# Optimization experiments

Measured on AMD Instinct MI355X. Metric: run time of the kernel, lower is better.

The kernel has to match this reference:

```python
import jax, jax.numpy as jnp
import numpy as np

N_NODES = 100000
N_EDGES = 1600000
D = 128  # conv_channels = [128, 128, 128] -> two GCNConv layers


def setup_inputs() -> dict:
    key = jax.random.key(0)
    ks = jax.random.split(key, 6)
    x = jax.random.normal(ks[0], (N_NODES, D), dtype=jnp.float32)
    edge_index = jax.random.randint(ks[1], (2, N_EDGES), 0, N_NODES, dtype=jnp.int32)
    s = 1.0 / np.sqrt(D)
    W1 = jax.random.uniform(ks[2], (D, D), jnp.float32, -s, s)
    b1 = jnp.zeros((D,), jnp.float32)
    W2 = jax.random.uniform(ks[3], (D, D), jnp.float32, -s, s)
    b2 = jnp.zeros((D,), jnp.float32)
    return {"x": x, "edge_index": edge_index, "W1": W1, "b1": b1, "W2": W2, "b2": b2}


def _gcn_layer(x, W, b, src, dst, norm, n_nodes):
    h = x @ W                       # [N, out]
    msg = h[src] * norm[:, None]    # gather + scale, [E', out]
    agg = jax.ops.segment_sum(msg, dst, num_segments=n_nodes)
    return agg + b


def reference(x, edge_index, W1, b1, W2, b2):
    n = x.shape[0]
    # add_self_loops: append (i, i) for every node
    loop = jnp.arange(n, dtype=edge_index.dtype)
    src = jnp.concatenate([edge_index[0], loop])
    dst = jnp.concatenate([edge_index[1], loop])
    # symmetric GCN normalization: deg over target nodes (unit edge weights)
    deg = jax.ops.segment_sum(jnp.ones_like(src, dtype=x.dtype), dst, num_segments=n)
    dis = jnp.where(deg > 0, jax.lax.rsqrt(deg), 0.0)
    norm = dis[src] * dis[dst]      # [E']

    h = _gcn_layer(x, W1, b1, src, dst, norm, n)
    h = jax.nn.elu(h)
    # dropout p=0.3 is identity in eval mode
    h = _gcn_layer(h, W2, b2, src, dst, norm, n)
    h = jax.nn.elu(h)
    return h
```

## Files before the change

### kernel.cpp

```cpp
#include <hip/hip_runtime.h>
#include <math.h>

#define NN 100000
#define NE 1600000
#define NT (NE + NN)
#define DD 128
#define NB 500
#define BR 200
#define BCAP 4096
#define NCH 2048
#define NBK 782
#define NBG 1563
#define BMAGIC 21474837u

typedef unsigned int uint;
typedef unsigned short ushort;
typedef __attribute__((ext_vector_type(8))) short bf16x8;
typedef __attribute__((ext_vector_type(4))) float f32x4;

__device__ __forceinline__ uint bfr(float f){
  uint u = __float_as_uint(f);
  return (u + 0x7FFFu + ((u >> 16) & 1u)) >> 16;
}
__device__ __forceinline__ uint pk2(float a, float b){
  return (bfr(a) & 0xFFFFu) | (bfr(b) << 16);
}
__device__ __forceinline__ bf16x8 asbf(uint4 u){
  union { uint4 u; bf16x8 b; } c; c.u = u; return c.b;
}


__global__ __launch_bounds__(256) void k_bucket(const int* __restrict__ ei,
    int* __restrict__ gcnt, uint* __restrict__ bedge){
  __shared__ uint   ent[NCH];
  __shared__ ushort bbs[NCH];
  __shared__ int    hist[NB];
  __shared__ int    fl[NB];
  __shared__ int    gb[NB];
  int t = threadIdx.x;
  int base = blockIdx.x * NCH;
  int nv = NE - base; if (nv > NCH) nv = NCH;
  for (int b = t; b < NB; b += 256){ hist[b] = 0; fl[b] = 0; }
  __syncthreads();
  for (int j = t; j < nv; j += 256){
    int i = base + j;
    uint s = (uint)ei[i];
    uint d = (uint)ei[NE + i];
    uint b = __umulhi(d, BMAGIC);
    uint dl = d - b*BR;
    ent[j] = s | (dl << 17);
    bbs[j] = (ushort)b;
    atomicAdd(&hist[b], 1);
  }
  __syncthreads();
  for (int b = t; b < NB; b += 256){
    int h = hist[b];
    gb[b] = h ? atomicAdd(&gcnt[b*16], h) : 0;
  }
  __syncthreads();
  for (int j = t; j < nv; j += 256){
    uint b = bbs[j];
    int q = atomicAdd(&fl[b], 1);
    bedge[(size_t)b*BCAP + gb[b] + q] = ent[j];
  }
}

__global__ __launch_bounds__(512) void k_bscan(const int* __restrict__ gcnt, int* __restrict__ bbase){
  __shared__ int s[512];
  int t = threadIdx.x;
  int v = (t < NB) ? (gcnt[t*16] + BR) : 0;
  s[t] = v;
  __syncthreads();
  for (int off = 1; off < 512; off <<= 1){
    int a = (t >= off) ? s[t-off] : 0;
    __syncthreads();
    s[t] += a;
    __syncthreads();
  }
  if (t < NB) bbase[t] = s[t] - v;
}

__global__ __launch_bounds__(256) void k_build(const int* __restrict__ gcnt,
    const int* __restrict__ bbase, const uint* __restrict__ bedge,
    float* __restrict__ dis, int* __restrict__ rowptr, uint* __restrict__ es){
  __shared__ uint eL[BCAP];
  __shared__ int  cl[BR];
  __shared__ int  fl[BR];
  __shared__ int  pf[256];
  int b = blockIdx.x, t = threadIdx.x;
  int base = bbase[b];
  if (t < BR){ cl[t] = 0; fl[t] = 0; }
  __syncthreads();
  int cnt = gcnt[b*16];
  for (int e = t; e < cnt; e += 256){
    uint u = bedge[(size_t)b*BCAP + e];
    eL[e] = u;
    atomicAdd(&cl[u >> 17], 1);
  }
  __syncthreads();
  int v = (t < BR) ? (cl[t] + 1) : 0;
  pf[t] = v;
  __syncthreads();
  for (int off = 1; off < 256; off <<= 1){
    int a = (t >= off) ? pf[t-off] : 0;
    __syncthreads();
    pf[t] += a;
    __syncthreads();
  }
  if (t < BR){
    int n  = b*BR + t;
    int p0 = base + pf[t] - v;
    rowptr[n] = p0;
    dis[n] = rsqrtf((float)(cl[t] + 1));
    es[p0 + cl[t]] = (uint)n;
  }
  if (b == NB-1 && t == 0) rowptr[NN] = NT;
  __syncthreads();
  for (int e = t; e < cnt; e += 256){
    uint u = eL[e];
    int  dloc = u >> 17;
    int  q  = atomicAdd(&fl[dloc], 1);
    int  p0 = base + pf[dloc] - (cl[dloc] + 1);
    es[p0 + q] = u & 0x1FFFFu;
  }
}

__global__ __launch_bounds__(256) void k_wt(const float* __restrict__ W1f, const float* __restrict__ W2f,
    uint* __restrict__ Wt1, uint* __restrict__ Wt2){
  const float* W = blockIdx.x ? W2f : W1f;
  uint* Wt = blockIdx.x ? Wt2 : Wt1;
  int t = threadIdx.x;
  int n = t >> 1, k0 = (t & 1) * 64;
  for (int kk = 0; kk < 64; kk += 2){
    float v0 = W[(size_t)(k0+kk  )*DD + n];
    float v1 = W[(size_t)(k0+kk+1)*DD + n];
    Wt[(size_t)n*64 + ((k0+kk)>>1)] = pk2(v0, v1);
  }
}

template<int IN_BF16>
__global__ __launch_bounds__(256) void k_gemm(const void* __restrict__ Xv,
    const uint* __restrict__ Wt, const float* __restrict__ dis,
    uint* __restrict__ Y, int nrows){
  int t = threadIdx.x;
  int wv = t >> 6, l = t & 63;
  int g = l >> 4, li = l & 15;
  int r = blockIdx.x*64 + wv*16 + li;
  bool valid = (r < nrows);

  f32x4 acc[8];
  #pragma unroll
  for (int i = 0; i < 8; ++i) acc[i] = (f32x4){0.f,0.f,0.f,0.f};

  #pragma unroll
  for (int ks = 0; ks < 4; ++ks){
    int k0 = ks*32 + g*8;
    uint4 xb;
    if (IN_BF16){
      xb = valid ? ((const uint4*)Xv)[(size_t)r*16 + (k0>>3)] : make_uint4(0,0,0,0);
    } else {
      if (valid){
        const float* X = (const float*)Xv;
        float4 f0 = ((const float4*)X)[(size_t)r*32 + (k0>>2)];
        float4 f1 = ((const float4*)X)[(size_t)r*32 + (k0>>2) + 1];
        xb.x = pk2(f0.x, f0.y); xb.y = pk2(f0.z, f0.w);
        xb.z = pk2(f1.x, f1.y); xb.w = pk2(f1.z, f1.w);
      } else xb = make_uint4(0,0,0,0);
    }
    bf16x8 bfrag = asbf(xb);
    #pragma unroll
    for (int nt = 0; nt < 8; ++nt){
      uint4 wa = ((const uint4*)Wt)[(size_t)(nt*16 + li)*16 + (k0>>3)];
      acc[nt] = __builtin_amdgcn_mfma_f32_16x16x32_bf16(asbf(wa), bfrag, acc[nt], 0, 0, 0);
    }
  }
  if (valid){
    float dr = dis[r];
    #pragma unroll
    for (int nt = 0; nt < 8; ++nt){
      uint2 o;
      o.x = pk2(acc[nt][0]*dr, acc[nt][1]*dr);
      o.y = pk2(acc[nt][2]*dr, acc[nt][3]*dr);
      *(uint2*)&Y[(size_t)r*64 + nt*8 + g*2] = o;
    }
  }
}

template<int OUT_BF16>
__global__ __launch_bounds__(256) void k_agg(const uint* __restrict__ H,
    const int* __restrict__ rowptr, const float* __restrict__ dis,
    const uint* __restrict__ es, const float* __restrict__ bias,
    void* __restrict__ outv){
  int wid  = threadIdx.x >> 6;
  int lane = threadIdx.x & 63;
  int n = blockIdx.x*4 + wid;
  int e0 = rowptr[n];
  int e1 = rowptr[n+1];
  float a0 = 0.f, a1 = 0.f, a2 = 0.f, a3 = 0.f;
  int e = e0;

#define ASTEP(k,A,B) { uint s##k = es[e+k]; \
    uint h##k = H[(size_t)s##k*64 + lane]; \
    A += __uint_as_float(h##k << 16); \
    B += __uint_as_float(h##k & 0xFFFF0000u); }

  for (; e + 16 <= e1; e += 16){
    ASTEP( 0,a0,a1) ASTEP( 1,a2,a3) ASTEP( 2,a0,a1) ASTEP( 3,a2,a3)
    ASTEP( 4,a0,a1) ASTEP( 5,a2,a3) ASTEP( 6,a0,a1) ASTEP( 7,a2,a3)
    ASTEP( 8,a0,a1) ASTEP( 9,a2,a3) ASTEP(10,a0,a1) ASTEP(11,a2,a3)
    ASTEP(12,a0,a1) ASTEP(13,a2,a3) ASTEP(14,a0,a1) ASTEP(15,a2,a3)
  }
  for (; e + 4 <= e1; e += 4){
    ASTEP(0,a0,a1) ASTEP(1,a2,a3) ASTEP(2,a0,a1) ASTEP(3,a2,a3)
  }
  for (; e < e1; ++e){
    ASTEP(0,a0,a1)
  }
#undef ASTEP

  float dn = dis[n];
  float2 b = *(const float2*)&bias[lane*2];
  float v0 = fmaf(dn, a0 + a2, b.x);
  float v1 = fmaf(dn, a1 + a3, b.y);
  v0 = (v0 > 0.f) ? v0 : expm1f(v0);
  v1 = (v1 > 0.f) ? v1 : expm1f(v1);
  if (OUT_BF16){
    ((uint*)outv)[(size_t)n*64 + lane] = pk2(v0, v1);
  } else {
    float2 o; o.x = v0; o.y = v1;
    *(float2*)&((float*)outv)[(size_t)n*DD + lane*2] = o;
  }
}


extern "C" void kernel_launch(void* const* d_in, const int* in_sizes, int n_in,
                              void* d_out, int out_size, void* d_ws, size_t ws_size,
                              hipStream_t stream){
  const float* x  = (const float*)d_in[0];
  const int*   ei = (const int*)d_in[1];
  const float* W1 = (const float*)d_in[2];
  const float* b1 = (const float*)d_in[3];
  const float* W2 = (const float*)d_in[4];
  const float* b2 = (const float*)d_in[5];

  int*   ws_i   = (int*)d_ws;
  int*   gcnt   = ws_i + 0;
  int*   bbase  = ws_i + 8000;
  float* dis    = (float*)(ws_i + 8576);
  int*   rowptr = ws_i + 108608;
  uint*  Wt1    = (uint*)(ws_i + 208704);
  uint*  Wt2    = (uint*)(ws_i + 216896);
  uint*  es     = (uint*)(ws_i + 225088);
  uint*  H      = (uint*)(ws_i + 1925120);
  uint*  bedge  = H;
  uint*  out1   = (uint*)(ws_i + 8325120);

  hipMemsetAsync(gcnt, 0, 8000*sizeof(int), stream);

  k_wt    <<<2,   256, 0, stream>>>(W1, W2, Wt1, Wt2);
  k_bucket<<<NBK, 256, 0, stream>>>(ei, gcnt, bedge);
  k_bscan <<<1,   512, 0, stream>>>(gcnt, bbase);
  k_build <<<NB,  256, 0, stream>>>(gcnt, bbase, bedge, dis, rowptr, es);

  k_gemm<0><<<NBG,   256, 0, stream>>>(x, Wt1, dis, H, NN);
  k_agg<1> <<<25000, 256, 0, stream>>>(H, rowptr, dis, es, b1, out1);
  k_gemm<1><<<NBG,   256, 0, stream>>>(out1, Wt2, dis, H, NN);
  k_agg<0> <<<25000, 256, 0, stream>>>(H, rowptr, dis, es, b2, d_out);
}
```

Baseline: 280.7 us.

## Fuse layer-1 aggregation with layer-2 GEMM and fold memset into init kernel

The first aggregation and the second feature transform are merged into one kernel. It gathers and aggregates 16 nodes per block into shared memory, applies bias and ELU, then runs the 128x128 MFMA on that tile and writes the scaled bf16 result directly. This removes the bf16 intermediate write and re-read and one kernel launch. The gcnt zeroing memset is also folded into the weight-transpose kernel to drop one API call. In exchange, each wave now processes 4 nodes serially, and the extra sync and shared-memory use may reduce gather parallelism.

```diff
diff --git a/kernel.cpp b/kernel.cpp
--- a/kernel.cpp
+++ b/kernel.cpp
@@ -29,6 +29,23 @@
   union { uint4 u; bf16x8 b; } c; c.u = u; return c.b;
 }
 
+__global__ __launch_bounds__(256) void k_init(const float* __restrict__ W1f, const float* __restrict__ W2f,
+    uint* __restrict__ Wt1, uint* __restrict__ Wt2, int* __restrict__ gcnt){
+  int t = threadIdx.x;
+  if (blockIdx.x == 2){
+    for (int i = t; i < 8000; i += 256) gcnt[i] = 0;
+    return;
+  }
+  const float* W = blockIdx.x ? W2f : W1f;
+  uint* Wt = blockIdx.x ? Wt2 : Wt1;
+  int n = t >> 1, k0 = (t & 1) * 64;
+  for (int kk = 0; kk < 64; kk += 2){
+    float v0 = W[(size_t)(k0+kk  )*DD + n];
+    float v1 = W[(size_t)(k0+kk+1)*DD + n];
+    Wt[(size_t)n*64 + ((k0+kk)>>1)] = pk2(v0, v1);
+  }
+}
+
 
 __global__ __launch_bounds__(256) void k_bucket(const int* __restrict__ ei,
     int* __restrict__ gcnt, uint* __restrict__ bedge){
@@ -125,21 +142,7 @@
   }
 }
 
-__global__ __launch_bounds__(256) void k_wt(const float* __restrict__ W1f, const float* __restrict__ W2f,
-    uint* __restrict__ Wt1, uint* __restrict__ Wt2){
-  const float* W = blockIdx.x ? W2f : W1f;
-  uint* Wt = blockIdx.x ? Wt2 : Wt1;
-  int t = threadIdx.x;
-  int n = t >> 1, k0 = (t & 1) * 64;
-  for (int kk = 0; kk < 64; kk += 2){
-    float v0 = W[(size_t)(k0+kk  )*DD + n];
-    float v1 = W[(size_t)(k0+kk+1)*DD + n];
-    Wt[(size_t)n*64 + ((k0+kk)>>1)] = pk2(v0, v1);
-  }
-}
-
-template<int IN_BF16>
-__global__ __launch_bounds__(256) void k_gemm(const void* __restrict__ Xv,
+__global__ __launch_bounds__(256) void k_gemm(const float* __restrict__ X,
     const uint* __restrict__ Wt, const float* __restrict__ dis,
     uint* __restrict__ Y, int nrows){
   int t = threadIdx.x;
@@ -156,17 +159,12 @@
   for (int ks = 0; ks < 4; ++ks){
     int k0 = ks*32 + g*8;
     uint4 xb;
-    if (IN_BF16){
-      xb = valid ? ((const uint4*)Xv)[(size_t)r*16 + (k0>>3)] : make_uint4(0,0,0,0);
-    } else {
-      if (valid){
-        const float* X = (const float*)Xv;
-        float4 f0 = ((const float4*)X)[(size_t)r*32 + (k0>>2)];
-        float4 f1 = ((const float4*)X)[(size_t)r*32 + (k0>>2) + 1];
-        xb.x = pk2(f0.x, f0.y); xb.y = pk2(f0.z, f0.w);
-        xb.z = pk2(f1.x, f1.y); xb.w = pk2(f1.z, f1.w);
-      } else xb = make_uint4(0,0,0,0);
-    }
+    if (valid){
+      float4 f0 = ((const float4*)X)[(size_t)r*32 + (k0>>2)];
+      float4 f1 = ((const float4*)X)[(size_t)r*32 + (k0>>2) + 1];
+      xb.x = pk2(f0.x, f0.y); xb.y = pk2(f0.z, f0.w);
+      xb.z = pk2(f1.x, f1.y); xb.w = pk2(f1.z, f1.w);
+    } else xb = make_uint4(0,0,0,0);
     bf16x8 bfrag = asbf(xb);
     #pragma unroll
     for (int nt = 0; nt < 8; ++nt){
@@ -184,6 +182,77 @@
       *(uint2*)&Y[(size_t)r*64 + nt*8 + g*2] = o;
     }
   }
+}
+
+__global__ __launch_bounds__(256) void k_aggemm(const uint* __restrict__ H,
+    const int* __restrict__ rowptr, const float* __restrict__ dis,
+    const uint* __restrict__ es, const float* __restrict__ bias,
+    const uint* __restrict__ Wt, uint* __restrict__ H2){
+  __shared__ float act[16][132];
+  int t = threadIdx.x;
+  int wv = t >> 6, lane = t & 63;
+  int n0 = blockIdx.x * 16;
+  float2 bb = *(const float2*)&bias[lane*2];
+
+  for (int j = 0; j < 4; ++j){
+    int n = n0 + wv*4 + j;
+    int e0 = rowptr[n], e1 = rowptr[n+1];
+    float a0 = 0.f, a1 = 0.f, a2 = 0.f, a3 = 0.f;
+    int e = e0;
+#define GSTEP(k,A,B) { uint s##k = es[e+k]; \
+    uint h##k = H[(size_t)s##k*64 + lane]; \
+    A += __uint_as_float(h##k << 16); \
+    B += __uint_as_float(h##k & 0xFFFF0000u); }
+    for (; e + 16 <= e1; e += 16){
+      GSTEP( 0,a0,a1) GSTEP( 1,a2,a3) GSTEP( 2,a0,a1) GSTEP( 3,a2,a3)
+      GSTEP( 4,a0,a1) GSTEP( 5,a2,a3) GSTEP( 6,a0,a1) GSTEP( 7,a2,a3)
+      GSTEP( 8,a0,a1) GSTEP( 9,a2,a3) GSTEP(10,a0,a1) GSTEP(11,a2,a3)
+      GSTEP(12,a0,a1) GSTEP(13,a2,a3) GSTEP(14,a0,a1) GSTEP(15,a2,a3)
+    }
+    for (; e + 4 <= e1; e += 4){
+      GSTEP(0,a0,a1) GSTEP(1,a2,a3) GSTEP(2,a0,a1) GSTEP(3,a2,a3)
+    }
+    for (; e < e1; ++e){
+      GSTEP(0,a0,a1)
+    }
+#undef GSTEP
+    float dn = dis[n];
+    float v0 = fmaf(dn, a0 + a2, bb.x);
+    float v1 = fmaf(dn, a1 + a3, bb.y);
+    v0 = (v0 > 0.f) ? v0 : expm1f(v0);
+    v1 = (v1 > 0.f) ? v1 : expm1f(v1);
+    act[wv*4 + j][lane*2]     = v0;
+    act[wv*4 + j][lane*2 + 1] = v1;
+  }
+  __syncthreads();
+
+  int g = lane >> 4, li = lane & 15;
+  int nid = n0 + li;
+  f32x4 acc0 = (f32x4){0.f,0.f,0.f,0.f};
+  f32x4 acc1 = (f32x4){0.f,0.f,0.f,0.f};
+  #pragma unroll
+  for (int ks = 0; ks < 4; ++ks){
+    int k0 = ks*32 + g*8;
+    float4 f0 = *(const float4*)&act[li][k0];
+    float4 f1 = *(const float4*)&act[li][k0 + 4];
+    uint4 xb;
+    xb.x = pk2(f0.x, f0.y); xb.y = pk2(f0.z, f0.w);
+    xb.z = pk2(f1.x, f1.y); xb.w = pk2(f1.z, f1.w);
+    bf16x8 bfrag = asbf(xb);
+    int nt0 = wv*2;
+    uint4 wa0 = ((const uint4*)Wt)[(size_t)(nt0*16 + li)*16 + (k0>>3)];
+    uint4 wa1 = ((const uint4*)Wt)[(size_t)((nt0+1)*16 + li)*16 + (k0>>3)];
+    acc0 = __builtin_amdgcn_mfma_f32_16x16x32_bf16(asbf(wa0), bfrag, acc0, 0, 0, 0);
+    acc1 = __builtin_amdgcn_mfma_f32_16x16x32_bf16(asbf(wa1), bfrag, acc1, 0, 0, 0);
+  }
+  float dr = dis[nid];
+  uint2 o;
+  o.x = pk2(acc0[0]*dr, acc0[1]*dr);
+  o.y = pk2(acc0[2]*dr, acc0[3]*dr);
+  *(uint2*)&H2[(size_t)nid*64 + (wv*2)*8 + g*2] = o;
+  o.x = pk2(acc1[0]*dr, acc1[1]*dr);
+  o.y = pk2(acc1[2]*dr, acc1[3]*dr);
+  *(uint2*)&H2[(size_t)nid*64 + (wv*2+1)*8 + g*2] = o;
 }
 
 template<int OUT_BF16>
@@ -253,17 +322,14 @@
   uint*  es     = (uint*)(ws_i + 225088);
   uint*  H      = (uint*)(ws_i + 1925120);
   uint*  bedge  = H;
-  uint*  out1   = (uint*)(ws_i + 8325120);
-
-  hipMemsetAsync(gcnt, 0, 8000*sizeof(int), stream);
-
-  k_wt    <<<2,   256, 0, stream>>>(W1, W2, Wt1, Wt2);
+  uint*  H2     = (uint*)(ws_i + 8325120);
+
+  k_init  <<<3,   256, 0, stream>>>(W1, W2, Wt1, Wt2, gcnt);
   k_bucket<<<NBK, 256, 0, stream>>>(ei, gcnt, bedge);
   k_bscan <<<1,   512, 0, stream>>>(gcnt, bbase);
   k_build <<<NB,  256, 0, stream>>>(gcnt, bbase, bedge, dis, rowptr, es);
 
-  k_gemm<0><<<NBG,   256, 0, stream>>>(x, Wt1, dis, H, NN);
-  k_agg<1> <<<25000, 256, 0, stream>>>(H, rowptr, dis, es, b1, out1);
-  k_gemm<1><<<NBG,   256, 0, stream>>>(out1, Wt2, dis, H, NN);
-  k_agg<0> <<<25000, 256, 0, stream>>>(H, rowptr, dis, es, b2, d_out);
-}
+  k_gemm  <<<NBG,  256, 0, stream>>>(x, Wt1, dis, H, NN);
+  k_aggemm<<<6250, 256, 0, stream>>>(H, rowptr, dis, es, b1, Wt2, H2);
+  k_agg<0><<<25000,256, 0, stream>>>(H2, rowptr, dis, es, b2, d_out);
+}
```

New measurement: 271.0 us. 1.04x faster.

## Slice H into feature-column panels and aggregate per slice with edge-parallel lanes

Applied to the files above, without the earlier changes.

The GEMM now writes its bf16 output in 8 column slices of 16 features each (32 bytes per node per slice) rather than row-major 256-byte rows. Aggregation launches a 2D grid over (node group, slice), and within each wave 8 edges are gathered in parallel by lane groups, then reduced with cross-lane shuffles. The intent is to shrink each slice's working set so gathers hit L2/MALL better and more edges are in flight per wave. The cost is 8x more blocks that each reread rowptr and es, and smaller 32-byte gathers. The weight transpose and the counter zeroing are also merged into one init kernel, replacing the memset.

```diff
diff --git a/kernel.cpp b/kernel.cpp
--- a/kernel.cpp
+++ b/kernel.cpp
@@ -11,6 +11,7 @@
 #define NCH 2048
 #define NBK 782
 #define NBG 1563
+#define SLN 800000
 #define BMAGIC 21474837u
 
 typedef unsigned int uint;
@@ -27,6 +28,23 @@
 }
 __device__ __forceinline__ bf16x8 asbf(uint4 u){
   union { uint4 u; bf16x8 b; } c; c.u = u; return c.b;
+}
+
+__global__ __launch_bounds__(256) void k_init(const float* __restrict__ W1f, const float* __restrict__ W2f,
+    uint* __restrict__ Wt1, uint* __restrict__ Wt2, int* __restrict__ gcnt){
+  int t = threadIdx.x;
+  if (blockIdx.x == 2){
+    for (int i = t; i < 8000; i += 256) gcnt[i] = 0;
+    return;
+  }
+  const float* W = blockIdx.x ? W2f : W1f;
+  uint* Wt = blockIdx.x ? Wt2 : Wt1;
+  int n = t >> 1, k0 = (t & 1) * 64;
+  for (int kk = 0; kk < 64; kk += 2){
+    float v0 = W[(size_t)(k0+kk  )*DD + n];
+    float v1 = W[(size_t)(k0+kk+1)*DD + n];
+    Wt[(size_t)n*64 + ((k0+kk)>>1)] = pk2(v0, v1);
+  }
 }
 
 
@@ -122,19 +140,6 @@
     int  q  = atomicAdd(&fl[dloc], 1);
     int  p0 = base + pf[dloc] - (cl[dloc] + 1);
     es[p0 + q] = u & 0x1FFFFu;
-  }
-}
-
-__global__ __launch_bounds__(256) void k_wt(const float* __restrict__ W1f, const float* __restrict__ W2f,
-    uint* __restrict__ Wt1, uint* __restrict__ Wt2){
-  const float* W = blockIdx.x ? W2f : W1f;
-  uint* Wt = blockIdx.x ? Wt2 : Wt1;
-  int t = threadIdx.x;
-  int n = t >> 1, k0 = (t & 1) * 64;
-  for (int kk = 0; kk < 64; kk += 2){
-    float v0 = W[(size_t)(k0+kk  )*DD + n];
-    float v1 = W[(size_t)(k0+kk+1)*DD + n];
-    Wt[(size_t)n*64 + ((k0+kk)>>1)] = pk2(v0, v1);
   }
 }
 
@@ -181,54 +186,61 @@
       uint2 o;
       o.x = pk2(acc[nt][0]*dr, acc[nt][1]*dr);
       o.y = pk2(acc[nt][2]*dr, acc[nt][3]*dr);
-      *(uint2*)&Y[(size_t)r*64 + nt*8 + g*2] = o;
+      *(uint2*)&Y[(size_t)nt*SLN + (size_t)r*8 + g*2] = o;
     }
   }
 }
 
 template<int OUT_BF16>
-__global__ __launch_bounds__(256) void k_agg(const uint* __restrict__ H,
+__global__ __launch_bounds__(256) void k_agg(const uint* __restrict__ Hs,
     const int* __restrict__ rowptr, const float* __restrict__ dis,
     const uint* __restrict__ es, const float* __restrict__ bias,
     void* __restrict__ outv){
-  int wid  = threadIdx.x >> 6;
-  int lane = threadIdx.x & 63;
-  int n = blockIdx.x*4 + wid;
-  int e0 = rowptr[n];
-  int e1 = rowptr[n+1];
-  float a0 = 0.f, a1 = 0.f, a2 = 0.f, a3 = 0.f;
+  int t = threadIdx.x;
+  int wv = t >> 6, l = t & 63;
+  int u = l & 7, eg = l >> 3;
+  int s = blockIdx.y;
+  int n = blockIdx.x*4 + wv;
+  const uint* Hsl = Hs + (size_t)s*SLN;
+  int e0 = rowptr[n], e1 = rowptr[n+1];
+  float a0 = 0.f, a1 = 0.f, b0 = 0.f, b1 = 0.f;
   int e = e0;
-
-#define ASTEP(k,A,B) { uint s##k = es[e+k]; \
-    uint h##k = H[(size_t)s##k*64 + lane]; \
-    A += __uint_as_float(h##k << 16); \
-    B += __uint_as_float(h##k & 0xFFFF0000u); }
-
   for (; e + 16 <= e1; e += 16){
-    ASTEP( 0,a0,a1) ASTEP( 1,a2,a3) ASTEP( 2,a0,a1) ASTEP( 3,a2,a3)
-    ASTEP( 4,a0,a1) ASTEP( 5,a2,a3) ASTEP( 6,a0,a1) ASTEP( 7,a2,a3)
-    ASTEP( 8,a0,a1) ASTEP( 9,a2,a3) ASTEP(10,a0,a1) ASTEP(11,a2,a3)
-    ASTEP(12,a0,a1) ASTEP(13,a2,a3) ASTEP(14,a0,a1) ASTEP(15,a2,a3)
-  }
-  for (; e + 4 <= e1; e += 4){
-    ASTEP(0,a0,a1) ASTEP(1,a2,a3) ASTEP(2,a0,a1) ASTEP(3,a2,a3)
-  }
-  for (; e < e1; ++e){
-    ASTEP(0,a0,a1)
-  }
-#undef ASTEP
-
+    uint sA = es[e + eg];
+    uint sB = es[e + 8 + eg];
+    uint hA = Hsl[(size_t)sA*8 + u];
+    uint hB = Hsl[(size_t)sB*8 + u];
+    a0 += __uint_as_float(hA << 16); a1 += __uint_as_float(hA & 0xFFFF0000u);
+    b0 += __uint_as_float(hB << 16); b1 += __uint_as_float(hB & 0xFFFF0000u);
+  }
+  if (e + 8 <= e1){
+    uint sA = es[e + eg];
+    uint hA = Hsl[(size_t)sA*8 + u];
+    a0 += __uint_as_float(hA << 16); a1 += __uint_as_float(hA & 0xFFFF0000u);
+    e += 8;
+  }
+  if (eg < e1 - e){
+    uint sA = es[e + eg];
+    uint hA = Hsl[(size_t)sA*8 + u];
+    b0 += __uint_as_float(hA << 16); b1 += __uint_as_float(hA & 0xFFFF0000u);
+  }
+  a0 += b0; a1 += b1;
+  a0 += __shfl_xor(a0, 8, 64);  a1 += __shfl_xor(a1, 8, 64);
+  a0 += __shfl_xor(a0, 16, 64); a1 += __shfl_xor(a1, 16, 64);
+  a0 += __shfl_xor(a0, 32, 64); a1 += __shfl_xor(a1, 32, 64);
   float dn = dis[n];
-  float2 b = *(const float2*)&bias[lane*2];
-  float v0 = fmaf(dn, a0 + a2, b.x);
-  float v1 = fmaf(dn, a1 + a3, b.y);
+  float2 bb = *(const float2*)&bias[s*16 + u*2];
+  float v0 = fmaf(dn, a0, bb.x);
+  float v1 = fmaf(dn, a1, bb.y);
   v0 = (v0 > 0.f) ? v0 : expm1f(v0);
   v1 = (v1 > 0.f) ? v1 : expm1f(v1);
-  if (OUT_BF16){
-    ((uint*)outv)[(size_t)n*64 + lane] = pk2(v0, v1);
-  } else {
-    float2 o; o.x = v0; o.y = v1;
-    *(float2*)&((float*)outv)[(size_t)n*DD + lane*2] = o;
+  if (eg == 0){
+    if (OUT_BF16){
+      ((uint*)outv)[(size_t)n*64 + s*8 + u] = pk2(v0, v1);
+    } else {
+      float2 o; o.x = v0; o.y = v1;
+      *(float2*)&((float*)outv)[(size_t)n*DD + s*16 + u*2] = o;
+    }
   }
 }
 
@@ -251,19 +263,18 @@
   uint*  Wt1    = (uint*)(ws_i + 208704);
   uint*  Wt2    = (uint*)(ws_i + 216896);
   uint*  es     = (uint*)(ws_i + 225088);
-  uint*  H      = (uint*)(ws_i + 1925120);
-  uint*  bedge  = H;
-  uint*  out1   = (uint*)(ws_i + 8325120);
-
-  hipMemsetAsync(gcnt, 0, 8000*sizeof(int), stream);
-
-  k_wt    <<<2,   256, 0, stream>>>(W1, W2, Wt1, Wt2);
+  uint*  bedge  = (uint*)(ws_i + 1925120);
+  uint*  out1   = (uint*)(ws_i + 1925120);
+  uint*  H      = (uint*)(ws_i + 8325120);
+  uint*  H2     = H;
+
+  k_init  <<<3,   256, 0, stream>>>(W1, W2, Wt1, Wt2, gcnt);
   k_bucket<<<NBK, 256, 0, stream>>>(ei, gcnt, bedge);
   k_bscan <<<1,   512, 0, stream>>>(gcnt, bbase);
   k_build <<<NB,  256, 0, stream>>>(gcnt, bbase, bedge, dis, rowptr, es);
 
-  k_gemm<0><<<NBG,   256, 0, stream>>>(x, Wt1, dis, H, NN);
-  k_agg<1> <<<25000, 256, 0, stream>>>(H, rowptr, dis, es, b1, out1);
-  k_gemm<1><<<NBG,   256, 0, stream>>>(out1, Wt2, dis, H, NN);
-  k_agg<0> <<<25000, 256, 0, stream>>>(H, rowptr, dis, es, b2, d_out);
-}
+  k_gemm<0><<<NBG, 256, 0, stream>>>(x, Wt1, dis, H, NN);
+  k_agg<1> <<<dim3(25000, 8), 256, 0, stream>>>(H, rowptr, dis, es, b1, out1);
+  k_gemm<1><<<NBG, 256, 0, stream>>>(out1, Wt2, dis, H2, NN);
+  k_agg<0> <<<dim3(25000, 8), 256, 0, stream>>>(H2, rowptr, dis, es, b2, d_out);
+}
```

Result: slower. 612.6 us (+118.2%).

## Stage GEMM weight and input tiles in padded shared memory; fold memset into init kernel

Applied to the files above, without the earlier changes.

The GEMM kernel now loads the full bf16 weight matrix and the block's 64-row input tile into padded LDS with coalesced vector loads, then reads the MFMA fragments from LDS. Previously each wave fetched strided fragments from global memory. The hipMemset of the bucket counters is folded into a combined weight-transpose/init kernel, saving one launch. Workspace buffers are also reassigned so out1 aliases the bedge scratch, and launch bounds request 3 blocks per CU, at the cost of about 52KB of LDS per block plus an extra barrier.

```diff
diff --git a/kernel.cpp b/kernel.cpp
--- a/kernel.cpp
+++ b/kernel.cpp
@@ -11,6 +11,7 @@
 #define NCH 2048
 #define NBK 782
 #define NBG 1563
+#define PW 68
 #define BMAGIC 21474837u
 
 typedef unsigned int uint;
@@ -27,6 +28,23 @@
 }
 __device__ __forceinline__ bf16x8 asbf(uint4 u){
   union { uint4 u; bf16x8 b; } c; c.u = u; return c.b;
+}
+
+__global__ __launch_bounds__(256) void k_init(const float* __restrict__ W1f, const float* __restrict__ W2f,
+    uint* __restrict__ Wt1, uint* __restrict__ Wt2, int* __restrict__ gcnt){
+  int t = threadIdx.x;
+  if (blockIdx.x == 2){
+    for (int i = t; i < 8000; i += 256) gcnt[i] = 0;
+    return;
+  }
+  const float* W = blockIdx.x ? W2f : W1f;
+  uint* Wt = blockIdx.x ? Wt2 : Wt1;
+  int n = t >> 1, k0 = (t & 1) * 64;
+  for (int kk = 0; kk < 64; kk += 2){
+    float v0 = W[(size_t)(k0+kk  )*DD + n];
+    float v1 = W[(size_t)(k0+kk+1)*DD + n];
+    Wt[(size_t)n*64 + ((k0+kk)>>1)] = pk2(v0, v1);
+  }
 }
 
 
@@ -125,56 +143,67 @@
   }
 }
 
-__global__ __launch_bounds__(256) void k_wt(const float* __restrict__ W1f, const float* __restrict__ W2f,
-    uint* __restrict__ Wt1, uint* __restrict__ Wt2){
-  const float* W = blockIdx.x ? W2f : W1f;
-  uint* Wt = blockIdx.x ? Wt2 : Wt1;
-  int t = threadIdx.x;
-  int n = t >> 1, k0 = (t & 1) * 64;
-  for (int kk = 0; kk < 64; kk += 2){
-    float v0 = W[(size_t)(k0+kk  )*DD + n];
-    float v1 = W[(size_t)(k0+kk+1)*DD + n];
-    Wt[(size_t)n*64 + ((k0+kk)>>1)] = pk2(v0, v1);
-  }
-}
-
 template<int IN_BF16>
-__global__ __launch_bounds__(256) void k_gemm(const void* __restrict__ Xv,
+__global__ __launch_bounds__(256, 3) void k_gemm(const void* __restrict__ Xv,
     const uint* __restrict__ Wt, const float* __restrict__ dis,
     uint* __restrict__ Y, int nrows){
-  int t = threadIdx.x;
+  __shared__ uint Ws[128*PW];
+  __shared__ uint Xs[64*PW];
+  int t = threadIdx.x;
+  int row0 = blockIdx.x * 64;
+
+  #pragma unroll
+  for (int it = 0; it < 8; ++it){
+    int f = it*256 + t;
+    uint4 v = ((const uint4*)Wt)[f];
+    int row = f >> 4, c4 = f & 15;
+    *(uint4*)&Ws[row*PW + c4*4] = v;
+  }
+  if (!IN_BF16){
+    const float* X = (const float*)Xv;
+    #pragma unroll
+    for (int it = 0; it < 8; ++it){
+      int f = it*256 + t;
+      int row = f >> 5, c4 = f & 31;
+      int gr = row0 + row;
+      float4 v = (gr < nrows) ? ((const float4*)X)[(size_t)gr*32 + c4]
+                              : make_float4(0.f,0.f,0.f,0.f);
+      uint2 p; p.x = pk2(v.x, v.y); p.y = pk2(v.z, v.w);
+      *(uint2*)&Xs[row*PW + c4*2] = p;
+    }
+  } else {
+    const uint* X = (const uint*)Xv;
+    #pragma unroll
+    for (int it = 0; it < 4; ++it){
+      int f = it*256 + t;
+      int row = f >> 4, c4 = f & 15;
+      int gr = row0 + row;
+      uint4 v = (gr < nrows) ? ((const uint4*)X)[(size_t)gr*16 + c4]
+                             : make_uint4(0,0,0,0);
+      *(uint4*)&Xs[row*PW + c4*4] = v;
+    }
+  }
+  __syncthreads();
+
   int wv = t >> 6, l = t & 63;
   int g = l >> 4, li = l & 15;
-  int r = blockIdx.x*64 + wv*16 + li;
-  bool valid = (r < nrows);
-
+  int rb = wv*16 + li;
+  int r  = row0 + rb;
   f32x4 acc[8];
   #pragma unroll
   for (int i = 0; i < 8; ++i) acc[i] = (f32x4){0.f,0.f,0.f,0.f};
 
   #pragma unroll
   for (int ks = 0; ks < 4; ++ks){
-    int k0 = ks*32 + g*8;
-    uint4 xb;
-    if (IN_BF16){
-      xb = valid ? ((const uint4*)Xv)[(size_t)r*16 + (k0>>3)] : make_uint4(0,0,0,0);
-    } else {
-      if (valid){
-        const float* X = (const float*)Xv;
-        float4 f0 = ((const float4*)X)[(size_t)r*32 + (k0>>2)];
-        float4 f1 = ((const float4*)X)[(size_t)r*32 + (k0>>2) + 1];
-        xb.x = pk2(f0.x, f0.y); xb.y = pk2(f0.z, f0.w);
-        xb.z = pk2(f1.x, f1.y); xb.w = pk2(f1.z, f1.w);
-      } else xb = make_uint4(0,0,0,0);
-    }
-    bf16x8 bfrag = asbf(xb);
+    int c = (ks*4 + g)*4;
+    bf16x8 bfrag = asbf(*(const uint4*)&Xs[rb*PW + c]);
     #pragma unroll
     for (int nt = 0; nt < 8; ++nt){
-      uint4 wa = ((const uint4*)Wt)[(size_t)(nt*16 + li)*16 + (k0>>3)];
-      acc[nt] = __builtin_amdgcn_mfma_f32_16x16x32_bf16(asbf(wa), bfrag, acc[nt], 0, 0, 0);
-    }
-  }
-  if (valid){
+      bf16x8 afrag = asbf(*(const uint4*)&Ws[(nt*16 + li)*PW + c]);
+      acc[nt] = __builtin_amdgcn_mfma_f32_16x16x32_bf16(afrag, bfrag, acc[nt], 0, 0, 0);
+    }
+  }
+  if (r < nrows){
     float dr = dis[r];
     #pragma unroll
     for (int nt = 0; nt < 8; ++nt){
@@ -251,19 +280,18 @@
   uint*  Wt1    = (uint*)(ws_i + 208704);
   uint*  Wt2    = (uint*)(ws_i + 216896);
   uint*  es     = (uint*)(ws_i + 225088);
-  uint*  H      = (uint*)(ws_i + 1925120);
-  uint*  bedge  = H;
-  uint*  out1   = (uint*)(ws_i + 8325120);
-
-  hipMemsetAsync(gcnt, 0, 8000*sizeof(int), stream);
-
-  k_wt    <<<2,   256, 0, stream>>>(W1, W2, Wt1, Wt2);
+  uint*  bedge  = (uint*)(ws_i + 1925120);
+  uint*  out1   = (uint*)(ws_i + 1925120);
+  uint*  H      = (uint*)(ws_i + 8325120);
+  uint*  H2     = H;
+
+  k_init  <<<3,   256, 0, stream>>>(W1, W2, Wt1, Wt2, gcnt);
   k_bucket<<<NBK, 256, 0, stream>>>(ei, gcnt, bedge);
   k_bscan <<<1,   512, 0, stream>>>(gcnt, bbase);
   k_build <<<NB,  256, 0, stream>>>(gcnt, bbase, bedge, dis, rowptr, es);
 
-  k_gemm<0><<<NBG,   256, 0, stream>>>(x, Wt1, dis, H, NN);
+  k_gemm<0><<<NBG, 256, 0, stream>>>(x, Wt1, dis, H, NN);
   k_agg<1> <<<25000, 256, 0, stream>>>(H, rowptr, dis, es, b1, out1);
-  k_gemm<1><<<NBG,   256, 0, stream>>>(out1, Wt2, dis, H, NN);
-  k_agg<0> <<<25000, 256, 0, stream>>>(H, rowptr, dis, es, b2, d_out);
-}
+  k_gemm<1><<<NBG, 256, 0, stream>>>(out1, Wt2, dis, H2, NN);
+  k_agg<0> <<<25000, 256, 0, stream>>>(H2, rowptr, dis, es, b2, d_out);
+}
```

Result: faster. 243.3 us (-13.4%).
